# Performance work log

Measured on AMD Instinct MI355X. Metric: run time of the kernel, lower is better.

Reference implementation:

```python
import jax, jax.numpy as jnp
import numpy as np

D_MODEL, D_STATE, D_CONV, EXPAND = 1024, 16, 4, 2
D_INNER = EXPAND * D_MODEL            # 2048
DT_RANK = int(np.ceil(D_MODEL / 16))  # 64
B, L = 2, 2048


def _dt_bias(key):
    # matches torch init: dt ~ exp(U(log dt_min, log dt_max)), inv via softplus inverse
    dt = jnp.exp(jax.random.uniform(key, (D_INNER,)) * (np.log(0.1) - np.log(0.001)) + np.log(0.001))
    dt = jnp.clip(dt, 1e-4, None)
    return dt + jnp.log(-jnp.expm1(-dt))


def _A_log():
    return jnp.log(jnp.tile(jnp.arange(1, D_STATE + 1, dtype=jnp.float32)[None, :], (D_INNER, 1)))


def setup_inputs() -> dict:
    key = jax.random.key(0)
    ks = jax.random.split(key, 16)
    n = lambda k, shape, s=0.02: jax.random.normal(k, shape, jnp.float32) * s
    return {
        "hidden_states": jax.random.normal(ks[0], (B, L, D_MODEL), jnp.float32),
        "in_proj_w": n(ks[1], (2 * D_INNER, D_MODEL)),
        "conv_w": n(ks[2], (D_INNER, 1, D_CONV), 0.2),
        "conv_b": jnp.zeros((D_INNER,), jnp.float32),
        "x_proj_w": n(ks[3], (DT_RANK + 2 * D_STATE, D_INNER)),
        "dt_proj_w": n(ks[4], (D_INNER, DT_RANK), 0.1),
        "dt_proj_b": _dt_bias(ks[5]),
        "A_log": _A_log(),
        "D": jnp.ones((D_INNER,), jnp.float32),
        "conv_w_b": n(ks[6], (D_INNER, 1, D_CONV), 0.2),
        "conv_b_b": jnp.zeros((D_INNER,), jnp.float32),
        "x_proj_w_b": n(ks[7], (DT_RANK + 2 * D_STATE, D_INNER)),
        "dt_proj_w_b": n(ks[8], (D_INNER, DT_RANK), 0.1),
        "dt_proj_b_b": _dt_bias(ks[9]),
        "A_b_log": _A_log(),
        "D_b": jnp.ones((D_INNER,), jnp.float32),
        "out_proj_w": n(ks[10], (D_MODEL, D_INNER)),
    }


def _silu(x):
    return x * jax.nn.sigmoid(x)


def _causal_dw_conv(x, w, b):
    # x: (B, Di, L); w: (Di, 1, K) depthwise; left-pad K-1 => causal, output length L
    y = jax.lax.conv_general_dilated(
        x, w, window_strides=(1,), padding=[(D_CONV - 1, 0)],
        dimension_numbers=("NCH", "OIH", "NCH"), feature_group_count=x.shape[1])
    return y + b[None, :, None]


def _mamba_branch(xz, conv_w, conv_b, x_proj_w, dt_proj_w, dt_proj_b, A_log, Dp):
    # xz: (B, 2*Di, L) -> y: (B, Di, L); selective scan (mamba_inner_fn_no_out_proj)
    x, z = jnp.split(xz, 2, axis=1)
    x = _silu(_causal_dw_conv(x, conv_w, conv_b))                       # (B,Di,L)
    x_dbl = jnp.einsum('rd,bdl->brl', x_proj_w, x)
    dt_r, Bc, Cc = jnp.split(x_dbl, [DT_RANK, DT_RANK + D_STATE], axis=1)
    delta = jax.nn.softplus(jnp.einsum('dr,brl->bdl', dt_proj_w, dt_r) + dt_proj_b[None, :, None])
    A = -jnp.exp(A_log)                                                 # (Di,N)

    def step(h, inp):
        d_t, u_t, b_t, c_t = inp   # (B,Di),(B,Di),(B,N),(B,N)
        h = h * jnp.exp(d_t[..., None] * A) + (d_t * u_t)[..., None] * b_t[:, None, :]
        return h, jnp.einsum('bdn,bn->bd', h, c_t)

    h0 = jnp.zeros((x.shape[0], D_INNER, D_STATE), x.dtype)
    xs = (jnp.moveaxis(delta, 2, 0), jnp.moveaxis(x, 2, 0),
          jnp.moveaxis(Bc, 2, 0), jnp.moveaxis(Cc, 2, 0))
    _, ys = jax.lax.scan(step, h0, xs)                                  # (L,B,Di)
    y = jnp.moveaxis(ys, 0, 2) + x * Dp[None, :, None]
    return y * _silu(z)


def reference(hidden_states, in_proj_w, conv_w, conv_b, x_proj_w, dt_proj_w, dt_proj_b,
              A_log, D, conv_w_b, conv_b_b, x_proj_w_b, dt_proj_w_b, dt_proj_b_b,
              A_b_log, D_b, out_proj_w):
    # bimamba_type == 'v2': forward scan + flipped backward scan, summed, then out_proj (no biases)
    xz = jnp.einsum('ed,bld->bel', in_proj_w, hidden_states)            # (B, 2*Di, L)
    out_f = _mamba_branch(xz, conv_w, conv_b, x_proj_w, dt_proj_w, dt_proj_b, A_log, D)
    out_r = _mamba_branch(xz[..., ::-1], conv_w_b, conv_b_b, x_proj_w_b,
                          dt_proj_w_b, dt_proj_b_b, A_b_log, D_b)[..., ::-1]
    y = out_f + out_r                                                   # (B,Di,L)
    return jnp.einsum('me,bel->blm', out_proj_w, y)                     # (B,L,D)
```

## Files before the change

kernel.cpp:

```cpp
#include <hip/hip_runtime.h>
#include <hip/hip_bf16.h>
#include <math.h>


#define L_SEQ  2048
#define B_SZ   2
#define DM     1024
#define DI     2048
#define NST    16
#define RTOT   96
#define DTR    64
#define NTOT   (B_SZ * L_SEQ)
#define ETOT   (2 * DI)
#define NCH    32
#define CHT    (L_SEQ / NCH)
#define SPLK   8

#define OFF_X    ((size_t)0)
#define OFF_ZT   (OFF_X   + (size_t)DI * NTOT)
#define OFF_XCF  (OFF_ZT  + (size_t)DI * NTOT)
#define OFF_XCB  (OFF_XCF + (size_t)DI * NTOT)
#define OFF_DLTB (OFF_XCB + (size_t)DI * NTOT)
#define OFF_XDF  (OFF_DLTB + (size_t)DI * NTOT)
#define OFF_XDB  (OFF_XDF + (size_t)RTOT * NTOT)
#define OFF_SS   (OFF_XDB + (size_t)RTOT * NTOT)
#define OFF_HL   (OFF_SS  + (size_t)4 * NCH * DI)
#define OFF_YGTF (OFF_HL  + (size_t)4 * NCH * NST * DI)
#define OFF_YGTB (OFF_YGTF + (size_t)NTOT * DI / 2)
#define OFF_XDT16F (OFF_YGTB + (size_t)NTOT * DI / 2)
#define OFF_XDT16B (OFF_XDT16F + (size_t)NTOT * DTR / 2)
#define OFF_DTW16F (OFF_XDT16B + (size_t)NTOT * DTR / 2)
#define OFF_DTW16B (OFF_DTW16F + (size_t)DI * DTR / 2)
#define WS_FLOATS  (OFF_DTW16B + (size_t)DI * DTR / 2)

typedef __bf16 bf16x8 __attribute__((ext_vector_type(8)));
typedef float  floatx4 __attribute__((ext_vector_type(4)));

__device__ __forceinline__ float silu_f(float x) {
    return x / (1.f + __expf(-x));
}

__device__ __forceinline__ void gl2lds16(const __bf16* g, __bf16* l) {
    __builtin_amdgcn_global_load_lds(
        (const __attribute__((address_space(1))) unsigned int*)g,
        (__attribute__((address_space(3))) unsigned int*)l, 16, 0, 0);
}

template<int MT, bool TRANS, bool SPLITZ>
__global__ __launch_bounds__(256)
void gemm_bf16(const __bf16* __restrict__ A, const __bf16* __restrict__ B,
               float* __restrict__ C, float* __restrict__ C2,
               int M, int N, int K)
{
    __shared__ __attribute__((aligned(16))) __bf16 As[MT * 32];
    __shared__ __attribute__((aligned(16))) __bf16 Bs[128 * 32];
    const int tid  = threadIdx.x;
    const int m0   = blockIdx.y * MT;
    const int n0   = blockIdx.x * 128;
    const int lane = tid & 63;
    const int wave = tid >> 6;
    const int wy   = wave >> 1, wx = wave & 1;
    const int lr   = lane & 15;
    const int q    = lane >> 4;
    constexpr int MF = MT / 32;

    floatx4 acc[MF][4];
#pragma unroll
    for (int i = 0; i < MF; ++i)
#pragma unroll
        for (int j = 0; j < 4; ++j) acc[i][j] = (floatx4)(0.0f);

    const int rl = lane >> 2;
    const int cp = lane & 3;
    const int sw = (q ^ ((lr >> 2) & 3)) * 8;

    for (int k0 = 0; k0 < K; k0 += 32) {
#pragma unroll
        for (int is = 0; is < MT / 64; ++is) {
            int r0  = wave * (MT / 4) + is * 16;
            int row = r0 + rl;
            int c   = cp ^ ((row >> 2) & 3);
            gl2lds16(A + (size_t)(m0 + row) * K + k0 + c * 8, &As[r0 * 32]);
        }
#pragma unroll
        for (int is = 0; is < 2; ++is) {
            int r0  = wave * 32 + is * 16;
            int row = r0 + rl;
            int c   = cp ^ ((row >> 2) & 3);
            gl2lds16(B + (size_t)(n0 + row) * K + k0 + c * 8, &Bs[r0 * 32]);
        }
        __syncthreads();

        bf16x8 af[MF], bfr[4];
#pragma unroll
        for (int i = 0; i < MF; ++i)
            af[i] = *(const bf16x8*)&As[(wy * (MT / 2) + i * 16 + lr) * 32 + sw];
#pragma unroll
        for (int j = 0; j < 4; ++j)
            bfr[j] = *(const bf16x8*)&Bs[(wx * 64 + j * 16 + lr) * 32 + sw];
#pragma unroll
        for (int i = 0; i < MF; ++i)
#pragma unroll
            for (int j = 0; j < 4; ++j)
                acc[i][j] = __builtin_amdgcn_mfma_f32_16x16x32_bf16(
                    af[i], bfr[j], acc[i][j], 0, 0, 0);
        __syncthreads();
    }

    const int mb = m0 + wy * (MT / 2);
    const int nb = n0 + wx * 64;
#pragma unroll
    for (int i = 0; i < MF; ++i) {
#pragma unroll
        for (int r = 0; r < 4; ++r) {
            int gm = mb + i * 16 + q * 4 + r;
#pragma unroll
            for (int j = 0; j < 4; ++j) {
                int gn = nb + j * 16 + lr;
                float val = acc[i][j][r];
                if constexpr (SPLITZ) {
                    if (m0 < DI) C[(size_t)gm * N + gn] = val;
                    else         C2[(size_t)gn * DI + (gm - DI)] = val;
                } else if constexpr (TRANS) {
                    C[(size_t)gn * M + gm] = val;
                } else {
                    C[(size_t)gm * N + gn] = val;
                }
            }
        }
    }
}

__global__ __launch_bounds__(256)
void dtproj_mfma(const __bf16* __restrict__ Af, const __bf16* __restrict__ Ab,
                 const __bf16* __restrict__ Bwf, const __bf16* __restrict__ Bwb,
                 const float* __restrict__ bif, const float* __restrict__ bib,
                 float* __restrict__ outf, float* __restrict__ outb)
{
    __shared__ __attribute__((aligned(16))) __bf16 As[128 * 32];
    __shared__ __attribute__((aligned(16))) __bf16 Bs[128 * 32];
    const int br = blockIdx.z;
    const __bf16* A  = br ? Ab : Af;
    const __bf16* B  = br ? Bwb : Bwf;
    const float*  bi = br ? bib : bif;
    float*        C  = br ? outb : outf;

    const int tid  = threadIdx.x;
    const int m0   = blockIdx.y * 128;
    const int n0   = blockIdx.x * 128;
    const int lane = tid & 63;
    const int wave = tid >> 6;
    const int wy   = wave >> 1, wx = wave & 1;
    const int lr   = lane & 15;
    const int q    = lane >> 4;

    floatx4 acc[4][4];
#pragma unroll
    for (int i = 0; i < 4; ++i)
#pragma unroll
        for (int j = 0; j < 4; ++j) acc[i][j] = (floatx4)(0.0f);

    const int rl = lane >> 2;
    const int cp = lane & 3;
    const int sw = (q ^ ((lr >> 2) & 3)) * 8;

#pragma unroll
    for (int k0 = 0; k0 < DTR; k0 += 32) {
#pragma unroll
        for (int is = 0; is < 2; ++is) {
            int r0  = wave * 32 + is * 16;
            int row = r0 + rl;
            int c   = cp ^ ((row >> 2) & 3);
            gl2lds16(A + (size_t)(m0 + row) * DTR + k0 + c * 8, &As[r0 * 32]);
            gl2lds16(B + (size_t)(n0 + row) * DTR + k0 + c * 8, &Bs[r0 * 32]);
        }
        __syncthreads();

        bf16x8 af[4], bfr[4];
#pragma unroll
        for (int i = 0; i < 4; ++i)
            af[i] = *(const bf16x8*)&As[(wy * 64 + i * 16 + lr) * 32 + sw];
#pragma unroll
        for (int j = 0; j < 4; ++j)
            bfr[j] = *(const bf16x8*)&Bs[(wx * 64 + j * 16 + lr) * 32 + sw];
#pragma unroll
        for (int i = 0; i < 4; ++i)
#pragma unroll
            for (int j = 0; j < 4; ++j)
                acc[i][j] = __builtin_amdgcn_mfma_f32_16x16x32_bf16(
                    af[i], bfr[j], acc[i][j], 0, 0, 0);
        __syncthreads();
    }

    const int mb = m0 + wy * 64;
    const int nb = n0 + wx * 64;
    float bj[4];
#pragma unroll
    for (int j = 0; j < 4; ++j) bj[j] = bi[nb + j * 16 + lr];
#pragma unroll
    for (int i = 0; i < 4; ++i) {
#pragma unroll
        for (int r = 0; r < 4; ++r) {
            int gm = mb + i * 16 + q * 4 + r;
#pragma unroll
            for (int j = 0; j < 4; ++j) {
                int gn = nb + j * 16 + lr;
                float x = acc[i][j][r] + bj[j];
                float o = (x > 20.f) ? x : __logf(1.f + __expf(x));
                C[(size_t)gm * DI + gn] = o;
            }
        }
    }
}

__global__ __launch_bounds__(256)
void cvt_bf16_k(const float* __restrict__ in, __bf16* __restrict__ out)
{
    const size_t i = ((size_t)blockIdx.x * 256 + threadIdx.x) * 8;
    float4 a = *(const float4*)(in + i);
    float4 b = *(const float4*)(in + i + 4);
    bf16x8 p;
    p[0]=(__bf16)a.x; p[1]=(__bf16)a.y; p[2]=(__bf16)a.z; p[3]=(__bf16)a.w;
    p[4]=(__bf16)b.x; p[5]=(__bf16)b.y; p[6]=(__bf16)b.z; p[7]=(__bf16)b.w;
    *(bf16x8*)(out + i) = p;
}

__global__ __launch_bounds__(256)
void addbf16_k(const __bf16* __restrict__ a, const __bf16* __restrict__ b,
               __bf16* __restrict__ o)
{
    const size_t i = ((size_t)blockIdx.x * 256 + threadIdx.x) * 8;
    bf16x8 x = *(const bf16x8*)(a + i);
    bf16x8 y = *(const bf16x8*)(b + i);
    bf16x8 s;
#pragma unroll
    for (int e = 0; e < 8; ++e) s[e] = (__bf16)((float)x[e] + (float)y[e]);
    *(bf16x8*)(o + i) = s;
}

__global__ __launch_bounds__(256)
void gemm_k3(const float* __restrict__ A, const float* __restrict__ Bm,
             float* __restrict__ C, int M, int N, int K)
{
    __shared__ float As[16][132];
    __shared__ float Bs[16][132];
    const int tid = threadIdx.x;
    const int n0 = blockIdx.x * 128;
    const int m0 = blockIdx.y * 128;
    int ksz  = K / (int)gridDim.z;
    int kbeg = blockIdx.z * ksz;
    int kend = kbeg + ksz;
    C += (size_t)blockIdx.z * M * N;
    const int tx = tid & 15, ty = tid >> 4;

    float acc[8][8];
#pragma unroll
    for (int i = 0; i < 8; ++i)
#pragma unroll
        for (int j = 0; j < 8; ++j) acc[i][j] = 0.f;

    for (int k0 = kbeg; k0 < kend; k0 += 16) {
#pragma unroll
        for (int it = 0; it < 2; ++it) {
            int i = tid + it * 256;
            int m = i >> 2, kq = i & 3;
            float4 v = make_float4(0.f, 0.f, 0.f, 0.f);
            int gm = m0 + m;
            if (gm < M) v = *(const float4*)(A + (size_t)gm * K + (k0 + kq * 4));
            As[kq * 4 + 0][m] = v.x; As[kq * 4 + 1][m] = v.y;
            As[kq * 4 + 2][m] = v.z; As[kq * 4 + 3][m] = v.w;
        }
#pragma unroll
        for (int it = 0; it < 2; ++it) {
            int i = tid + it * 256;
            int n = i >> 2, kq = i & 3;
            float4 v = *(const float4*)(Bm + (size_t)(n0 + n) * K + (k0 + kq * 4));
            Bs[kq * 4 + 0][n] = v.x; Bs[kq * 4 + 1][n] = v.y;
            Bs[kq * 4 + 2][n] = v.z; Bs[kq * 4 + 3][n] = v.w;
        }
        __syncthreads();
#pragma unroll
        for (int kk = 0; kk < 16; ++kk) {
            float av[8], bv[8];
            *(float4*)&av[0] = *(const float4*)&As[kk][ty * 8];
            *(float4*)&av[4] = *(const float4*)&As[kk][ty * 8 + 4];
            *(float4*)&bv[0] = *(const float4*)&Bs[kk][tx * 8];
            *(float4*)&bv[4] = *(const float4*)&Bs[kk][tx * 8 + 4];
#pragma unroll
            for (int i = 0; i < 8; ++i)
#pragma unroll
                for (int j = 0; j < 8; ++j)
                    acc[i][j] = fmaf(av[i], bv[j], acc[i][j]);
        }
        __syncthreads();
    }

#pragma unroll
    for (int i = 0; i < 8; ++i) {
        int gm = m0 + ty * 8 + i;
        if (gm < M) {
            float* cp = C + (size_t)gm * N + n0 + tx * 8;
            *(float4*)cp       = make_float4(acc[i][0], acc[i][1], acc[i][2], acc[i][3]);
            *(float4*)(cp + 4) = make_float4(acc[i][4], acc[i][5], acc[i][6], acc[i][7]);
        }
    }
}

__global__ __launch_bounds__(256)
void reduce8t_k(const float* __restrict__ P, float* __restrict__ out,
                __bf16* __restrict__ out2, size_t stride)
{
    const size_t i4 = ((size_t)blockIdx.x * 256 + threadIdx.x) * 4;
    float4 s = *(const float4*)(P + i4);
#pragma unroll
    for (int z = 1; z < SPLK; ++z) {
        float4 v = *(const float4*)(P + (size_t)z * stride + i4);
        s.x += v.x; s.y += v.y; s.z += v.z; s.w += v.w;
    }
    *(float4*)(out + i4) = s;
    const int r = (int)(i4 >> 12);
    if (r < DTR) {
        const int n = (int)(i4 & (NTOT - 1));
        out2[(size_t)(n + 0) * DTR + r] = (__bf16)s.x;
        out2[(size_t)(n + 1) * DTR + r] = (__bf16)s.y;
        out2[(size_t)(n + 2) * DTR + r] = (__bf16)s.z;
        out2[(size_t)(n + 3) * DTR + r] = (__bf16)s.w;
    }
}

__global__ __launch_bounds__(256)
void conv_k(const float* __restrict__ x,
            const float* __restrict__ wf, const float* __restrict__ bf,
            const float* __restrict__ wb, const float* __restrict__ bb,
            float* __restrict__ xcf, float* __restrict__ xcb)
{
    __shared__ float xs[70 * 65];
    const int tid = threadIdx.x;
    const int d0 = blockIdx.x * 64;
    const int n0 = blockIdx.y * 64;
    const int b  = n0 >> 11;
    const int l0 = n0 & (L_SEQ - 1);
    const size_t bbase = (size_t)b << 11;

    for (int i = tid; i < 64 * 70; i += 256) {
        int r = i / 70, c = i % 70;
        int l = l0 - 3 + c;
        float v = 0.f;
        if (l >= 0 && l < L_SEQ) v = x[(size_t)(d0 + r) * NTOT + bbase + l];
        xs[c * 65 + r] = v;
    }
    __syncthreads();

    const int dd = tid & 63;
    const int lq = tid >> 6;
    const int d  = d0 + dd;
    const float w0 = wf[d * 4 + 0], w1 = wf[d * 4 + 1];
    const float w2 = wf[d * 4 + 2], w3 = wf[d * 4 + 3];
    const float v0 = wb[d * 4 + 0], v1 = wb[d * 4 + 1];
    const float v2 = wb[d * 4 + 2], v3 = wb[d * 4 + 3];
    const float bfv = bf[d], bbv = bb[d];

    for (int lr = 0; lr < 64; lr += 4) {
        const int lo = lr + lq;
        const int l  = l0 + lo;
        float x0 = xs[(lo + 0) * 65 + dd];
        float x1 = xs[(lo + 1) * 65 + dd];
        float x2 = xs[(lo + 2) * 65 + dd];
        float x3 = xs[(lo + 3) * 65 + dd];
        float x4 = xs[(lo + 4) * 65 + dd];
        float x5 = xs[(lo + 5) * 65 + dd];
        float x6 = xs[(lo + 6) * 65 + dd];
        float xf = bfv + w0 * x0 + w1 * x1 + w2 * x2 + w3 * x3;
        xcf[((size_t)bbase + l) * DI + d] = silu_f(xf);
        float xb = bbv + v3 * x3 + v2 * x4 + v1 * x5 + v0 * x6;
        xcb[((size_t)bbase + (L_SEQ - 1 - l)) * DI + d] = silu_f(xb);
    }
}

__global__ __launch_bounds__(256)
void scan_part1(const float* __restrict__ xcf, const float* __restrict__ xcb,
                const float* __restrict__ xdf, const float* __restrict__ xdb,
                const float* __restrict__ dltf, const float* __restrict__ dltb,
                const float* __restrict__ Alog_f, const float* __restrict__ Alog_b,
                float* __restrict__ SS, float* __restrict__ HL)
{
    __shared__ float Bsh[NST][CHT];
    const int tid = threadIdx.x;
    const int d  = blockIdx.x * 256 + tid;
    const int c  = blockIdx.y;
    const int bb = blockIdx.z;
    const int b  = bb & 1;
    const int br = bb >> 1;

    const float* u    = br ? xcb : xcf;
    const float* dl   = br ? dltb : dltf;
    const float* xd   = br ? xdb : xdf;
    const float* Alog = br ? Alog_b : Alog_f;

    const size_t nbase = (size_t)b * L_SEQ + (size_t)c * CHT;
    const float* bcB = xd + (size_t)DTR * NTOT + nbase;

    for (int i = tid; i < NST * CHT; i += 256) {
        int n = i >> 6;
        int t = i & (CHT - 1);
        Bsh[n][t] = bcB[(size_t)n * NTOT + t];
    }

    float Arow[NST], h[NST];
#pragma unroll
    for (int n = 0; n < NST; ++n) {
        Arow[n] = -__expf(Alog[d * NST + n]);
        h[n] = 0.f;
    }
    float S = 0.f;

    const float* up = u  + nbase * DI + d;
    const float* dp = dl + nbase * DI + d;

    __syncthreads();

    float dv[4], uv[4];
#pragma unroll
    for (int k = 0; k < 4; ++k) {
        dv[k] = dp[(size_t)k * DI];
        uv[k] = up[(size_t)k * DI];
    }

    for (int tr = 0; tr < CHT; tr += 4) {
        float dvn[4], uvn[4];
#pragma unroll
        for (int k = 0; k < 4; ++k) {
            dvn[k] = dp[(size_t)(tr + 4 + k) * DI];
            uvn[k] = up[(size_t)(tr + 4 + k) * DI];
        }
        S += (dv[0] + dv[1]) + (dv[2] + dv[3]);
        float du[4] = { dv[0]*uv[0], dv[1]*uv[1], dv[2]*uv[2], dv[3]*uv[3] };
#pragma unroll
        for (int n = 0; n < NST; ++n) {
            float4 Bn = *(const float4*)&Bsh[n][tr];
            float hn = h[n];
            float An = Arow[n];
            hn = hn * __expf(dv[0] * An) + du[0] * Bn.x;
            hn = hn * __expf(dv[1] * An) + du[1] * Bn.y;
            hn = hn * __expf(dv[2] * An) + du[2] * Bn.z;
            hn = hn * __expf(dv[3] * An) + du[3] * Bn.w;
            h[n] = hn;
        }
#pragma unroll
        for (int k = 0; k < 4; ++k) { dv[k] = dvn[k]; uv[k] = uvn[k]; }
    }
    SS[((size_t)bb * NCH + c) * DI + d] = S;
#pragma unroll
    for (int n = 0; n < NST; ++n)
        HL[(((size_t)bb * NCH + c) * NST + n) * DI + d] = h[n];
}

__global__ __launch_bounds__(256)
void scan_part2(const float* __restrict__ SS, float* HL,
                const float* __restrict__ Alog_f, const float* __restrict__ Alog_b)
{
    const int d  = blockIdx.x * 256 + threadIdx.x;
    const int n  = blockIdx.y;
    const int bb = blockIdx.z;
    const int br = bb >> 1;
    const float* Alog = br ? Alog_b : Alog_f;
    const float A = -__expf(Alog[d * NST + n]);

    float H = 0.f;
#pragma unroll
    for (int c = 0; c < NCH; ++c) {
        const size_t si = ((size_t)bb * NCH + c) * DI + d;
        const size_t hi = (((size_t)bb * NCH + c) * NST + n) * DI + d;
        float hl = HL[hi];
        HL[hi] = H;
        H = __expf(SS[si] * A) * H + hl;
    }
}

__global__ __launch_bounds__(256)
void scan_part3(const float* __restrict__ zt,
                const float* __restrict__ xcf, const float* __restrict__ xcb,
                const float* __restrict__ xdf, const float* __restrict__ xdb,
                const float* __restrict__ dltf, const float* __restrict__ dltb,
                const float* __restrict__ HIN,
                __bf16* __restrict__ ygtf, __bf16* __restrict__ ygtb,
                const float* __restrict__ Alog_f, const float* __restrict__ Alog_b,
                const float* __restrict__ Df, const float* __restrict__ Db)
{
    __shared__ float BCs[2 * NST][CHT];
    const int tid = threadIdx.x;
    const int d  = blockIdx.x * 256 + tid;
    const int c  = blockIdx.y;
    const int bb = blockIdx.z;
    const int b  = bb & 1;
    const int br = bb >> 1;

    const float* u    = br ? xcb : xcf;
    const float* dl   = br ? dltb : dltf;
    const float* xd   = br ? xdb : xdf;
    const float* Alog = br ? Alog_b : Alog_f;
    const float* Dv   = br ? Db : Df;
    __bf16*      ygt  = br ? ygtb : ygtf;

    const size_t nbase = (size_t)b * L_SEQ + (size_t)c * CHT;
    const float* bcB = xd + (size_t)DTR * NTOT + nbase;

    for (int i = tid; i < 2 * NST * CHT; i += 256) {
        int n = i >> 6;
        int t = i & (CHT - 1);
        BCs[n][t] = bcB[(size_t)n * NTOT + t];
    }

    float Arow[NST], h[NST];
#pragma unroll
    for (int n = 0; n < NST; ++n) {
        Arow[n] = -__expf(Alog[d * NST + n]);
        h[n] = HIN[(((size_t)bb * NCH + c) * NST + n) * DI + d];
    }
    const float Dp = Dv[d];

    const float* up = u  + nbase * DI + d;
    const float* dp = dl + nbase * DI + d;
    const size_t bL = (size_t)b * L_SEQ;
    const int    t0 = c * CHT;

    __syncthreads();

    float dv[4], uv[4];
#pragma unroll
    for (int k = 0; k < 4; ++k) {
        dv[k] = dp[(size_t)k * DI];
        uv[k] = up[(size_t)k * DI];
    }

    for (int tr = 0; tr < CHT; tr += 4) {
        float dvn[4], uvn[4];
#pragma unroll
        for (int k = 0; k < 4; ++k) {
            dvn[k] = dp[(size_t)(tr + 4 + k) * DI];
            uvn[k] = up[(size_t)(tr + 4 + k) * DI];
        }
        size_t nn[4];
        float  zv[4];
#pragma unroll
        for (int k = 0; k < 4; ++k) {
            int t = t0 + tr + k;
            nn[k] = br ? (bL + (L_SEQ - 1 - t)) : (bL + t);
            zv[k] = zt[nn[k] * DI + d];
        }
        float du[4] = { dv[0]*uv[0], dv[1]*uv[1], dv[2]*uv[2], dv[3]*uv[3] };
        float y[4] = { 0.f, 0.f, 0.f, 0.f };
#pragma unroll
        for (int n = 0; n < NST; ++n) {
            float4 Bn = *(const float4*)&BCs[n][tr];
            float4 Cn = *(const float4*)&BCs[NST + n][tr];
            float hn = h[n];
            float An = Arow[n];
            hn = hn * __expf(dv[0] * An) + du[0] * Bn.x;  y[0] = fmaf(hn, Cn.x, y[0]);
            hn = hn * __expf(dv[1] * An) + du[1] * Bn.y;  y[1] = fmaf(hn, Cn.y, y[1]);
            hn = hn * __expf(dv[2] * An) + du[2] * Bn.z;  y[2] = fmaf(hn, Cn.z, y[2]);
            hn = hn * __expf(dv[3] * An) + du[3] * Bn.w;  y[3] = fmaf(hn, Cn.w, y[3]);
            h[n] = hn;
        }
#pragma unroll
        for (int k = 0; k < 4; ++k) {
            float yo = (y[k] + uv[k] * Dp) * silu_f(zv[k]);
            ygt[nn[k] * DI + d] = (__bf16)yo;
        }
#pragma unroll
        for (int k = 0; k < 4; ++k) { dv[k] = dvn[k]; uv[k] = uvn[k]; }
    }
}

extern "C" void kernel_launch(void* const* d_in, const int* in_sizes, int n_in,
                              void* d_out, int out_size, void* d_ws, size_t ws_size,
                              hipStream_t stream)
{
    const float* hid     = (const float*)d_in[0];
    const float* inw     = (const float*)d_in[1];
    const float* convw   = (const float*)d_in[2];
    const float* convb   = (const float*)d_in[3];
    const float* xpw     = (const float*)d_in[4];
    const float* dtw     = (const float*)d_in[5];
    const float* dtb     = (const float*)d_in[6];
    const float* Alog    = (const float*)d_in[7];
    const float* Dv      = (const float*)d_in[8];
    const float* convw_b = (const float*)d_in[9];
    const float* convb_b = (const float*)d_in[10];
    const float* xpw_b   = (const float*)d_in[11];
    const float* dtw_b   = (const float*)d_in[12];
    const float* dtb_b   = (const float*)d_in[13];
    const float* Alog_b  = (const float*)d_in[14];
    const float* Dv_b    = (const float*)d_in[15];
    const float* outw    = (const float*)d_in[16];
    float* out = (float*)d_out;
    float* ws  = (float*)d_ws;

    if (ws_size < WS_FLOATS * sizeof(float)) return;

    float*  X    = ws + OFF_X;
    float*  ZT   = ws + OFF_ZT;
    float*  XCF  = ws + OFF_XCF;
    float*  XCB  = ws + OFF_XCB;
    float*  DLTB = ws + OFF_DLTB;
    float*  XDF  = ws + OFF_XDF;
    float*  XDB  = ws + OFF_XDB;
    float*  SS   = ws + OFF_SS;
    float*  HLb  = ws + OFF_HL;
    __bf16* YGTF = (__bf16*)(ws + OFF_YGTF);
    __bf16* YGTB = (__bf16*)(ws + OFF_YGTB);
    float*  PF   = ws + OFF_YGTF;
    float*  PB   = ws + OFF_YGTB;
    float*  DLTF = X;
    __bf16* IW16 = (__bf16*)(ws + OFF_SS);
    __bf16* HD16 = IW16 + (size_t)ETOT * DM;
    __bf16* OW16 = (__bf16*)(ws + OFF_XCB);
    __bf16* YGS  = (__bf16*)(ws + OFF_XCF);
    __bf16* XDT16F = (__bf16*)(ws + OFF_XDT16F);
    __bf16* XDT16B = (__bf16*)(ws + OFF_XDT16B);
    __bf16* DTW16F = (__bf16*)(ws + OFF_DTW16F);
    __bf16* DTW16B = (__bf16*)(ws + OFF_DTW16B);

    dim3 blk(256);
    cvt_bf16_k<<<dim3(ETOT * DM / 2048), blk, 0, stream>>>(inw, IW16);
    cvt_bf16_k<<<dim3(NTOT * DM / 2048), blk, 0, stream>>>(hid, HD16);
    cvt_bf16_k<<<dim3(DI * DTR / 2048), blk, 0, stream>>>(dtw, DTW16F);
    cvt_bf16_k<<<dim3(DI * DTR / 2048), blk, 0, stream>>>(dtw_b, DTW16B);
    gemm_bf16<128, false, true><<<dim3(32, 32), blk, 0, stream>>>(
        IW16, HD16, X, ZT, ETOT, NTOT, DM);
    conv_k<<<dim3(32, 64), blk, 0, stream>>>(X, convw, convb, convw_b, convb_b, XCF, XCB);
    gemm_k3<<<dim3(32, 1, SPLK), blk, 0, stream>>>(xpw, XCF, PF, RTOT, NTOT, DI);
    gemm_k3<<<dim3(32, 1, SPLK), blk, 0, stream>>>(xpw_b, XCB, PB, RTOT, NTOT, DI);
    reduce8t_k<<<dim3(RTOT * NTOT / 1024), blk, 0, stream>>>(PF, XDF, XDT16F, (size_t)RTOT * NTOT);
    reduce8t_k<<<dim3(RTOT * NTOT / 1024), blk, 0, stream>>>(PB, XDB, XDT16B, (size_t)RTOT * NTOT);
    dtproj_mfma<<<dim3(DI / 128, NTOT / 128, 2), blk, 0, stream>>>(
        XDT16F, XDT16B, DTW16F, DTW16B, dtb, dtb_b, DLTF, DLTB);
    scan_part1<<<dim3(DI / 256, NCH, 4), blk, 0, stream>>>(
        XCF, XCB, XDF, XDB, DLTF, DLTB, Alog, Alog_b, SS, HLb);
    scan_part2<<<dim3(DI / 256, NST, 4), blk, 0, stream>>>(
        SS, HLb, Alog, Alog_b);
    scan_part3<<<dim3(DI / 256, NCH, 4), blk, 0, stream>>>(
        ZT, XCF, XCB, XDF, XDB, DLTF, DLTB, HLb, YGTF, YGTB, Alog, Alog_b, Dv, Dv_b);
    cvt_bf16_k<<<dim3(DM * DI / 2048), blk, 0, stream>>>(outw, OW16);
    addbf16_k<<<dim3(NTOT * DI / 2048), blk, 0, stream>>>(YGTF, YGTB, YGS);
    gemm_bf16<64, true, false><<<dim3(32, 16), blk, 0, stream>>>(
        OW16, YGS, out, nullptr, DM, NTOT, DI);

    (void)in_sizes; (void)n_in; (void)out_size;
}
```

Baseline: 502.4 us.

## Double-buffer LDS tiles in GEMMs and vectorize transposed epilogue stores

Converts the bf16 MFMA GEMM and dt-projection kernels to double-buffered LDS. The next K tile's global-to-LDS loads are issued before computing on the current tile, with explicit vmcnt waits and raw barriers in place of __syncthreads. The transposed and split-z epilogues now write each accumulator fragment as one float4 store instead of four scalar stores. LDS use doubles, and the hand-counted vmcnt literals depend on the exact number of loads per stage.

```diff
diff --git a/kernel.cpp b/kernel.cpp
--- a/kernel.cpp
+++ b/kernel.cpp
@@ -52,8 +52,9 @@
                float* __restrict__ C, float* __restrict__ C2,
                int M, int N, int K)
 {
-    __shared__ __attribute__((aligned(16))) __bf16 As[MT * 32];
-    __shared__ __attribute__((aligned(16))) __bf16 Bs[128 * 32];
+    static_assert(MT == 64 || MT == 128, "vmcnt literals assume MT in {64,128}");
+    __shared__ __attribute__((aligned(16))) __bf16 As[2][MT * 32];
+    __shared__ __attribute__((aligned(16))) __bf16 Bs[2][128 * 32];
     const int tid  = threadIdx.x;
     const int m0   = blockIdx.y * MT;
     const int n0   = blockIdx.x * 128;
@@ -74,37 +75,53 @@
     const int cp = lane & 3;
     const int sw = (q ^ ((lr >> 2) & 3)) * 8;
 
-    for (int k0 = 0; k0 < K; k0 += 32) {
+    auto stage = [&](int s, int k0) {
 #pragma unroll
         for (int is = 0; is < MT / 64; ++is) {
             int r0  = wave * (MT / 4) + is * 16;
             int row = r0 + rl;
             int c   = cp ^ ((row >> 2) & 3);
-            gl2lds16(A + (size_t)(m0 + row) * K + k0 + c * 8, &As[r0 * 32]);
+            gl2lds16(A + (size_t)(m0 + row) * K + k0 + c * 8, &As[s][r0 * 32]);
         }
 #pragma unroll
         for (int is = 0; is < 2; ++is) {
             int r0  = wave * 32 + is * 16;
             int row = r0 + rl;
             int c   = cp ^ ((row >> 2) & 3);
-            gl2lds16(B + (size_t)(n0 + row) * K + k0 + c * 8, &Bs[r0 * 32]);
-        }
-        __syncthreads();
+            gl2lds16(B + (size_t)(n0 + row) * K + k0 + c * 8, &Bs[s][r0 * 32]);
+        }
+    };
+
+    stage(0, 0);
+    int cur = 0;
+    for (int k0 = 0; k0 < K; k0 += 32) {
+        if (k0 + 32 < K) {
+            stage(cur ^ 1, k0 + 32);
+            if constexpr (MT == 128) {
+                asm volatile("s_waitcnt vmcnt(4)" ::: "memory");
+            } else {
+                asm volatile("s_waitcnt vmcnt(3)" ::: "memory");
+            }
+        } else {
+            asm volatile("s_waitcnt vmcnt(0)" ::: "memory");
+        }
+        __builtin_amdgcn_s_barrier();
 
         bf16x8 af[MF], bfr[4];
 #pragma unroll
         for (int i = 0; i < MF; ++i)
-            af[i] = *(const bf16x8*)&As[(wy * (MT / 2) + i * 16 + lr) * 32 + sw];
+            af[i] = *(const bf16x8*)&As[cur][(wy * (MT / 2) + i * 16 + lr) * 32 + sw];
 #pragma unroll
         for (int j = 0; j < 4; ++j)
-            bfr[j] = *(const bf16x8*)&Bs[(wx * 64 + j * 16 + lr) * 32 + sw];
+            bfr[j] = *(const bf16x8*)&Bs[cur][(wx * 64 + j * 16 + lr) * 32 + sw];
 #pragma unroll
         for (int i = 0; i < MF; ++i)
 #pragma unroll
             for (int j = 0; j < 4; ++j)
                 acc[i][j] = __builtin_amdgcn_mfma_f32_16x16x32_bf16(
                     af[i], bfr[j], acc[i][j], 0, 0, 0);
-        __syncthreads();
+        __builtin_amdgcn_s_barrier();
+        cur ^= 1;
     }
 
     const int mb = m0 + wy * (MT / 2);
@@ -112,20 +129,23 @@
 #pragma unroll
     for (int i = 0; i < MF; ++i) {
 #pragma unroll
-        for (int r = 0; r < 4; ++r) {
-            int gm = mb + i * 16 + q * 4 + r;
-#pragma unroll
-            for (int j = 0; j < 4; ++j) {
-                int gn = nb + j * 16 + lr;
-                float val = acc[i][j][r];
-                if constexpr (SPLITZ) {
-                    if (m0 < DI) C[(size_t)gm * N + gn] = val;
-                    else         C2[(size_t)gn * DI + (gm - DI)] = val;
-                } else if constexpr (TRANS) {
-                    C[(size_t)gn * M + gm] = val;
+        for (int j = 0; j < 4; ++j) {
+            int gn  = nb + j * 16 + lr;
+            int gm0 = mb + i * 16 + q * 4;
+            if constexpr (SPLITZ) {
+                if (m0 < DI) {
+#pragma unroll
+                    for (int r = 0; r < 4; ++r)
+                        C[(size_t)(gm0 + r) * N + gn] = acc[i][j][r];
                 } else {
-                    C[(size_t)gm * N + gn] = val;
+                    *(floatx4*)&C2[(size_t)gn * DI + (gm0 - DI)] = acc[i][j];
                 }
+            } else if constexpr (TRANS) {
+                *(floatx4*)&C[(size_t)gn * M + gm0] = acc[i][j];
+            } else {
+#pragma unroll
+                for (int r = 0; r < 4; ++r)
+                    C[(size_t)(gm0 + r) * N + gn] = acc[i][j][r];
             }
         }
     }
@@ -137,8 +157,8 @@
                  const float* __restrict__ bif, const float* __restrict__ bib,
                  float* __restrict__ outf, float* __restrict__ outb)
 {
-    __shared__ __attribute__((aligned(16))) __bf16 As[128 * 32];
-    __shared__ __attribute__((aligned(16))) __bf16 Bs[128 * 32];
+    __shared__ __attribute__((aligned(16))) __bf16 As[2][128 * 32];
+    __shared__ __attribute__((aligned(16))) __bf16 Bs[2][128 * 32];
     const int br = blockIdx.z;
     const __bf16* A  = br ? Ab : Af;
     const __bf16* B  = br ? Bwb : Bwf;
@@ -165,31 +185,37 @@
     const int sw = (q ^ ((lr >> 2) & 3)) * 8;
 
 #pragma unroll
-    for (int k0 = 0; k0 < DTR; k0 += 32) {
+    for (int t = 0; t < 2; ++t) {
+        int k0 = t * 32;
 #pragma unroll
         for (int is = 0; is < 2; ++is) {
             int r0  = wave * 32 + is * 16;
             int row = r0 + rl;
             int c   = cp ^ ((row >> 2) & 3);
-            gl2lds16(A + (size_t)(m0 + row) * DTR + k0 + c * 8, &As[r0 * 32]);
-            gl2lds16(B + (size_t)(n0 + row) * DTR + k0 + c * 8, &Bs[r0 * 32]);
-        }
-        __syncthreads();
+            gl2lds16(A + (size_t)(m0 + row) * DTR + k0 + c * 8, &As[t][r0 * 32]);
+            gl2lds16(B + (size_t)(n0 + row) * DTR + k0 + c * 8, &Bs[t][r0 * 32]);
+        }
+    }
+
+#pragma unroll
+    for (int t = 0; t < 2; ++t) {
+        if (t == 0) asm volatile("s_waitcnt vmcnt(4)" ::: "memory");
+        else        asm volatile("s_waitcnt vmcnt(0)" ::: "memory");
+        __builtin_amdgcn_s_barrier();
 
         bf16x8 af[4], bfr[4];
 #pragma unroll
         for (int i = 0; i < 4; ++i)
-            af[i] = *(const bf16x8*)&As[(wy * 64 + i * 16 + lr) * 32 + sw];
+            af[i] = *(const bf16x8*)&As[t][(wy * 64 + i * 16 + lr) * 32 + sw];
 #pragma unroll
         for (int j = 0; j < 4; ++j)
-            bfr[j] = *(const bf16x8*)&Bs[(wx * 64 + j * 16 + lr) * 32 + sw];
+            bfr[j] = *(const bf16x8*)&Bs[t][(wx * 64 + j * 16 + lr) * 32 + sw];
 #pragma unroll
         for (int i = 0; i < 4; ++i)
 #pragma unroll
             for (int j = 0; j < 4; ++j)
                 acc[i][j] = __builtin_amdgcn_mfma_f32_16x16x32_bf16(
                     af[i], bfr[j], acc[i][j], 0, 0, 0);
-        __syncthreads();
     }
 
     const int mb = m0 + wy * 64;
```

Result: faster. 482.0 us (-4.1%).
